# Optimization experiments

Measured on AMD Instinct MI355X. Metric: run time of the kernel, lower is better.

## Reference

```python
import jax, jax.numpy as jnp
import numpy as np

_MAX_SQRT_GRADIENT = 1000.0

@jax.custom_vjp
def sqrt_bound(x):
    return jnp.sqrt(x)

def _sb_fwd(x):
    return jnp.sqrt(x), x

def _sb_bwd(x, g):
    return (g / jnp.sqrt(jnp.maximum(4.0 * x, 1.0 / (_MAX_SQRT_GRADIENT ** 2))),)

sqrt_bound.defvjp(_sb_fwd, _sb_bwd)


def setup_inputs() -> dict:
    B, S, H, L, NH, K = 2, 4096, 2048, 2048, 16, 4
    BW = L // NH
    key = jax.random.key(0)
    ks = jax.random.split(key, 8)
    f = lambda k, shape: jax.random.normal(k, shape, dtype=jnp.float32) * 0.02
    return {
        "input_states": jax.random.normal(ks[0], (B, S, H), dtype=jnp.float32),
        "Wy": f(ks[1], (H, L)), "by": jnp.zeros((L,), jnp.float32),
        "Wx": f(ks[2], (H, L)), "bx": jnp.zeros((L,), jnp.float32),
        "conv_w": f(ks[3], (L, 1, K)), "conv_b": jnp.zeros((L,), jnp.float32),
        "rec_param": f(ks[4], (L,)),
        "igw": f(ks[5], (NH, BW, BW)), "igb": jnp.zeros((NH, BW), jnp.float32),
        "rgw": f(ks[6], (NH, BW, BW)), "rgb": jnp.zeros((NH, BW), jnp.float32),
        "Wout": f(ks[7], (L, H)), "bout": jnp.zeros((H,), jnp.float32),
        "position_ids": jnp.tile(jnp.arange(S, dtype=jnp.int32), (B, 1)),
    }


def reference(input_states, Wy, by, Wx, bx, conv_w, conv_b, rec_param,
              igw, igb, rgw, rgb, Wout, bout, position_ids):
    B, S, H = input_states.shape
    L = Wy.shape[1]
    NH, BW = igw.shape[0], igw.shape[1]
    K = conv_w.shape[-1]

    # y branch: linear + gelu
    y = jax.nn.gelu(input_states @ Wy + by)                      # [B,S,L]

    # x branch: linear + causal depthwise conv1d
    x = input_states @ Wx + bx                                    # [B,S,L]
    xc = jnp.transpose(x, (0, 2, 1))                              # [B,L,S]
    xc = jax.lax.conv_general_dilated(
        xc, conv_w, window_strides=(1,), padding=[(K - 1, 0)],
        dimension_numbers=("NCH", "OIH", "NCH"), feature_group_count=L)
    x = jnp.transpose(xc, (0, 2, 1)) + conv_b                     # [B,S,L]

    # RG-LRU block-diagonal gates
    xh = x.reshape(B, S, NH, BW)
    ig = jax.nn.sigmoid(jnp.einsum("bsnd,nde->bsne", xh, igw) + igb).reshape(B, S, L)
    rg = jax.nn.sigmoid(jnp.einsum("bsnd,nde->bsne", xh, rgw) + rgb).reshape(B, S, L)

    log_a = -8.0 * rg * jax.nn.softplus(rec_param)                # [B,S,L]
    a = jnp.exp(log_a)
    reset = (position_ids == 0)[:, :, None]                       # [B,S,1]

    mult = sqrt_bound(1.0 - jnp.exp(2.0 * log_a))
    mult = jnp.where(reset, 1.0, mult)
    normed = x * ig * mult                                        # [B,S,L]
    a_eff = jnp.where(reset, 0.0, a)                              # [B,S,L]

    def step(h, inp):
        a_t, x_t = inp
        h = a_t.astype(jnp.float32) * h + x_t.astype(jnp.float32)
        return h, h

    h0 = jnp.zeros((B, L), jnp.float32)
    _, hs = jax.lax.scan(step, h0,
                         (jnp.swapaxes(a_eff, 0, 1), jnp.swapaxes(normed, 0, 1)))
    hs = jnp.swapaxes(hs, 0, 1).astype(input_states.dtype)        # [B,S,L]

    return (hs * y) @ Wout + bout                                 # [B,S,H]
```

## Files before the change

### kernel.cpp

```cpp
#include <hip/hip_runtime.h>
#include <cstdint>
#include <cstddef>

#define B_  2
#define S_  4096
#define H_  2048
#define L_  2048
#define NH_ 16
#define M_  (B_*S_)
#define NC_ 64
#define CS_ 64

typedef unsigned short u16;
typedef short  bf8v  __attribute__((ext_vector_type(8)));
typedef u16    u16x8 __attribute__((ext_vector_type(8)));
typedef float  f32x4 __attribute__((ext_vector_type(4)));

__device__ __forceinline__ float bf2f(u16 u){
  union { unsigned i; float f; } v; v.i = ((unsigned)u) << 16; return v.f;
}
__device__ __forceinline__ u16 f2bf(float f){
  union { float f; unsigned i; } v; v.f = f;
  unsigned u = v.i;
  return (u16)((u + 0x7FFFu + ((u >> 16) & 1u)) >> 16);
}
__device__ __forceinline__ void gld16(const void* g, void* l){
  __builtin_amdgcn_global_load_lds((const __attribute__((address_space(1))) void*)g,
                                   (__attribute__((address_space(3))) void*)l, 16, 0, 0);
}

__global__ __launch_bounds__(256)
void gemm_bf16(const u16* __restrict__ A, int lda,
               const u16* __restrict__ Bt, int K,
               const float* __restrict__ bias1, const float* __restrict__ bias2,
               void* __restrict__ C1, u16* __restrict__ C2, int ldc,
               int gelu_flag, int f32out)
{
  __shared__ u16 Alds[128*64];
  __shared__ u16 Blds[128*64];
  const int t    = threadIdx.x;
  const int lane = t & 63;
  const int w    = t >> 6;
  const int wr   = w >> 1, wc = w & 1;
  const int lr   = lane & 15, lk = lane >> 4;

  const int nwg = gridDim.x * gridDim.y;
  const int bid = blockIdx.y * gridDim.x + blockIdx.x;
  const int cpx = nwg >> 3;
  const int swz = (bid & 7) * cpx + (bid >> 3);
  const int bx  = swz % gridDim.x;
  const int by  = swz / gridDim.x;

  const long rowA0 = (long)by * 128;
  const long colB0 = (long)bx * 128;
  const u16* Ag = A  + rowA0 * lda;
  const u16* Bg = Bt + colB0 * K;
  const int srow = t >> 3, scol = t & 7;

#define STAGE(KT) do {                                                     \
    _Pragma("unroll")                                                      \
    for (int it = 0; it < 4; ++it) {                                       \
      int r  = it*32 + srow;                                               \
      int ca = (scol ^ (r & 7)) * 8;                                       \
      gld16(Ag + (long)r*lda + (long)(KT)*64 + ca, Alds + it*2048 + t*8);  \
      gld16(Bg + (long)r*K   + (long)(KT)*64 + ca, Blds + it*2048 + t*8);  \
    } } while(0)

  f32x4 acc[4][4];
#pragma unroll
  for (int m=0;m<4;m++)
#pragma unroll
    for (int n=0;n<4;n++) acc[m][n] = (f32x4){0.f,0.f,0.f,0.f};

  const int nk = K / 64;
  STAGE(0);
  __syncthreads();

  for (int kt = 0; kt < nk; ++kt) {
    bf8v af[4][2], bv[4][2];
#pragma unroll
    for (int m=0;m<4;m++)
#pragma unroll
      for (int ks=0;ks<2;ks++){
        int r  = wr*64 + m*16 + lr;
        int kb = (ks*32 + lk*8)*2;
        af[m][ks] = *(const bf8v*)((const char*)Alds + r*128 + (kb ^ ((r&7)<<4)));
      }
#pragma unroll
    for (int n=0;n<4;n++)
#pragma unroll
      for (int ks=0;ks<2;ks++){
        int r  = wc*64 + n*16 + lr;
        int kb = (ks*32 + lk*8)*2;
        bv[n][ks] = *(const bf8v*)((const char*)Blds + r*128 + (kb ^ ((r&7)<<4)));
      }
    __syncthreads();
    if (kt + 1 < nk) STAGE(kt + 1);
    __builtin_amdgcn_sched_barrier(0);
#pragma unroll
    for (int ks=0;ks<2;ks++)
#pragma unroll
      for (int m=0;m<4;m++)
#pragma unroll
        for (int n=0;n<4;n++)
          acc[m][n] = __builtin_amdgcn_mfma_f32_16x16x32_bf16(af[m][ks], bv[n][ks], acc[m][n], 0, 0, 0);
    if (kt + 1 < nk) __syncthreads();
  }
#undef STAGE

  u16*   Cb = (u16*)C1;
  float* Cf = (float*)C1;
#pragma unroll
  for (int m=0;m<4;m++){
    long row = rowA0 + wr*64 + m*16 + lk*4;
#pragma unroll
    for (int n=0;n<4;n++){
      int col = (int)colB0 + wc*64 + n*16 + lr;
      bool sec = (C2 != nullptr) && (col >= L_);
      float bvv = sec ? bias2[col - L_] : bias1[col];
      bool gel = gelu_flag && !sec;
#pragma unroll
      for (int rr=0; rr<4; ++rr){
        float v = acc[m][n][rr] + bvv;
        if (gel) {
          float u  = 0.7978845608028654f * (v + 0.044715f * v*v*v);
          float tu = fminf(fmaxf(2.f*u, -80.f), 80.f);
          float e  = __expf(tu);
          float th = (e - 1.f) / (e + 1.f);
          v = 0.5f * v * (1.f + th);
        }
        if (sec)          C2[(row+rr)*(long)L_ + (col - L_)] = f2bf(v);
        else if (f32out)  Cf[(row+rr)*(long)ldc + col] = v;
        else              Cb[(row+rr)*(long)ldc + col] = f2bf(v);
      }
    }
  }
}

__global__ __launch_bounds__(256)
void gates_fused(const u16* __restrict__ Xlin, const float* __restrict__ cw,
                 const float* __restrict__ cb, const u16* __restrict__ Gt,
                 const float* __restrict__ gbias, const float* __restrict__ c8,
                 const int* __restrict__ pos,
                 u16* __restrict__ Ae, u16* __restrict__ Nr)
{
  __shared__ __align__(16) char sm[16384 + 32768];
  const int t  = threadIdx.x;
  const int sc = blockIdx.x;
  const int n  = blockIdx.y;
  const int b  = blockIdx.z;
  const int s0 = sc*64;
  const long rowg0 = (long)b*S_ + s0;

  char* xc = sm;
  u16*  xs = (u16*)(sm + 16384);
  char* bs = sm + 16384;

  for (int it=0; it<5; ++it){
    int slot = it*256 + t;
    if (slot < 67*16){
      int i = slot >> 4, c = slot & 15;
      int s = s0 - 3 + i;
      u16x8 v = (u16x8){0,0,0,0,0,0,0,0};
      if (s >= 0)
        v = *(const u16x8*)(Xlin + ((long)b*S_ + s)*L_ + n*128 + c*8);
      *(u16x8*)(xs + i*128 + c*8) = v;
    }
  }
  __syncthreads();

#pragma unroll
  for (int it=0; it<4; ++it){
    int slot = it*256 + t;
    int row = slot >> 4, c = slot & 15;
    int d0 = c*8;
    float a8[8];
#pragma unroll
    for (int j=0;j<8;j++) a8[j] = cb[n*128 + d0 + j];
#pragma unroll
    for (int k=0;k<4;k++){
      u16x8 xv = *(const u16x8*)(xs + (row+k)*128 + d0);
#pragma unroll
      for (int j=0;j<8;j++)
        a8[j] += bf2f(xv[j]) * cw[(n*128 + d0 + j)*4 + k];
    }
    u16x8 o;
#pragma unroll
    for (int j=0;j<8;j++) o[j] = f2bf(a8[j]);
    *(u16x8*)(xc + row*256 + ((d0*2) ^ ((row&7)<<4))) = o;
  }
  __syncthreads();

  const int w  = t >> 6;
  const int lane = t & 63;
  const int lr = lane & 15, lk = lane >> 4;
  const int arow = w*16 + lr;

  bf8v af[4];
#pragma unroll
  for (int ks=0;ks<4;ks++)
    af[ks] = *(const bf8v*)(xc + arow*256 + ((ks*64 + lk*16) ^ ((arow&7)<<4)));

  f32x4 aig[8], brg[8];
#pragma unroll
  for (int half=0; half<2; ++half){
#pragma unroll
    for (int it=0; it<8; ++it){
      int slot = it*256 + t;
      int jr = slot >> 4, c = slot & 15;
      gld16(Gt + (size_t)(n*256 + half*128 + jr)*128 + (size_t)((c ^ (jr&7))*8),
            bs + slot*16);
    }
    __syncthreads();
#pragma unroll
    for (int nf=0; nf<8; ++nf){
      f32x4 acc = (f32x4){0.f,0.f,0.f,0.f};
      int jrow = nf*16 + lr;
#pragma unroll
      for (int ks=0;ks<4;ks++){
        bf8v bv = *(const bf8v*)(bs + jrow*256 + ((ks*64 + lk*16) ^ ((jrow&7)<<4)));
        acc = __builtin_amdgcn_mfma_f32_16x16x32_bf16(af[ks], bv, acc, 0, 0, 0);
      }
      if (half==0) aig[nf] = acc; else brg[nf] = acc;
    }
    __syncthreads();
  }

#pragma unroll
  for (int rr=0; rr<4; ++rr){
    int row = w*16 + lk*4 + rr;
    long gs = rowg0 + row;
    bool reset = (pos[gs] == 0);
#pragma unroll
    for (int nf=0; nf<8; ++nf){
      int dl = nf*16 + lr;
      float ig = 1.f / (1.f + __expf(-(aig[nf][rr] + gbias[n*256 + dl])));
      float rg = 1.f / (1.f + __expf(-(brg[nf][rr] + gbias[n*256 + 128 + dl])));
      float la = c8[n*128 + dl] * rg;
      float a  = __expf(la);
      float mult = reset ? 1.f : sqrtf(fmaxf(1.f - __expf(2.f*la), 0.f));
      u16 xv = *(const u16*)(xc + row*256 + ((dl*2) ^ ((row&7)<<4)));
      float x = bf2f(xv);
      Nr[gs*L_ + n*128 + dl] = f2bf(x * ig * mult);
      Ae[gs*L_ + n*128 + dl] = f2bf(reset ? 0.f : a);
    }
  }
}

__global__ __launch_bounds__(256)
void transpose_cvt(const float* __restrict__ in, u16* __restrict__ out, int R, int C)
{
  __shared__ float tile[64][65];
  int t  = threadIdx.x;
  int tc = blockIdx.x * 64, tr = blockIdx.y * 64;
  int r  = t >> 2, c0 = (t & 3) * 16;
#pragma unroll
  for (int i=0;i<4;i++)
    *(f32x4*)(&tile[r][c0 + i*4]) = *(const f32x4*)(in + (long)(tr+r)*C + tc + c0 + i*4);
  __syncthreads();
  int nl = t >> 2;
#pragma unroll
  for (int it=0; it<2; ++it){
    int g = (t & 3) + it*4;
    u16x8 o;
#pragma unroll
    for (int e=0;e<8;e++) o[e] = f2bf(tile[g*8+e][nl]);
    *(u16x8*)(out + (long)(tc+nl)*R + tr + g*8) = o;
  }
}

__global__ __launch_bounds__(256)
void prep_small(const float* __restrict__ igw, const float* __restrict__ rgw,
                const float* __restrict__ igb, const float* __restrict__ rgb,
                const float* __restrict__ rec, u16* __restrict__ Gt,
                float* __restrict__ gbias, float* __restrict__ c8)
{
  int idx = blockIdx.x*256 + threadIdx.x;
  int d = idx & 127, g = idx >> 7;
  int n = g >> 8, j = g & 255;
  float v = (j < 128) ? igw[(n*128 + d)*128 + j] : rgw[(n*128 + d)*128 + (j-128)];
  Gt[idx] = f2bf(v);
  if (idx < NH_*256) {
    int nn = idx >> 8, jj = idx & 255;
    gbias[idx] = (jj < 128) ? igb[nn*128 + jj] : rgb[nn*128 + jj - 128];
  }
  if (idx < L_) c8[idx] = -8.f * log1pf(__expf(rec[idx]));
}

__global__ __launch_bounds__(256)
void cvt_x(const float* __restrict__ X, u16* __restrict__ Xb)
{
  long idx = (long)blockIdx.x*256 + threadIdx.x;
  f32x4 a = *(const f32x4*)(X + idx*8);
  f32x4 b = *(const f32x4*)(X + idx*8 + 4);
  u16x8 o;
#pragma unroll
  for (int e=0;e<4;e++){ o[e] = f2bf(a[e]); o[4+e] = f2bf(b[e]); }
  *(u16x8*)(Xb + idx*8) = o;
}

__global__ __launch_bounds__(256)
void scan1(const u16* __restrict__ Ae, const u16* __restrict__ Nr,
           float* __restrict__ Ach, float* __restrict__ Hch)
{
  int t = threadIdx.x;
  int l = (blockIdx.x & 7)*256 + t;
  int c = (blockIdx.x >> 3) & (NC_-1);
  int b = blockIdx.x >> 9;
  long base = ((long)b*S_ + (long)c*CS_)*L_ + l;
  float A = 1.f, h = 0.f;
#pragma unroll 8
  for (int s=0; s<CS_; ++s){
    float a = bf2f(Ae[base + (long)s*L_]);
    float x = bf2f(Nr[base + (long)s*L_]);
    h = fmaf(a, h, x);
    A *= a;
  }
  long o = ((long)b*NC_ + c)*L_ + l;
  Ach[o] = A; Hch[o] = h;
}

__global__ __launch_bounds__(256)
void scan2(const float* __restrict__ Ach, const float* __restrict__ Hch,
           float* __restrict__ Hcar)
{
  int idx = blockIdx.x*256 + threadIdx.x;
  int b = idx >> 11, l = idx & (L_-1);
  float h = 0.f;
  for (int c=0; c<NC_; ++c){
    long o = ((long)b*NC_ + c)*L_ + l;
    Hcar[o] = h;
    h = fmaf(Ach[o], h, Hch[o]);
  }
}

__global__ __launch_bounds__(256)
void scan3(const u16* __restrict__ Ae, const u16* __restrict__ Nr,
           const float* __restrict__ Hcar, const u16* __restrict__ Y,
           u16* __restrict__ Z)
{
  int t = threadIdx.x;
  int l = (blockIdx.x & 7)*256 + t;
  int c = (blockIdx.x >> 3) & (NC_-1);
  int b = blockIdx.x >> 9;
  long base = ((long)b*S_ + (long)c*CS_)*L_ + l;
  float h = Hcar[((long)b*NC_ + c)*L_ + l];
#pragma unroll 8
  for (int s=0; s<CS_; ++s){
    long o = base + (long)s*L_;
    h = fmaf(bf2f(Ae[o]), h, bf2f(Nr[o]));
    Z[o] = f2bf(h * bf2f(Y[o]));
  }
}

extern "C" void kernel_launch(void* const* d_in, const int* in_sizes, int n_in,
                              void* d_out, int out_size, void* d_ws, size_t ws_size,
                              hipStream_t stream)
{
  (void)in_sizes; (void)n_in; (void)out_size; (void)ws_size;
  const float* X    = (const float*)d_in[0];
  const float* Wy   = (const float*)d_in[1];
  const float* by   = (const float*)d_in[2];
  const float* Wx   = (const float*)d_in[3];
  const float* bx   = (const float*)d_in[4];
  const float* cw   = (const float*)d_in[5];
  const float* cb   = (const float*)d_in[6];
  const float* rec  = (const float*)d_in[7];
  const float* igw  = (const float*)d_in[8];
  const float* igb  = (const float*)d_in[9];
  const float* rgw  = (const float*)d_in[10];
  const float* rgb  = (const float*)d_in[11];
  const float* Wout = (const float*)d_in[12];
  const float* bout = (const float*)d_in[13];
  const int*   pos  = (const int*)d_in[14];
  float* out = (float*)d_out;

  char* ws = (char*)d_ws;
  size_t o_Xbf  = 0;
  size_t o_Xlin = o_Xbf  + (size_t)M_*H_*2;
  size_t o_WyT  = o_Xlin + (size_t)M_*L_*2;
  size_t o_WxT  = o_WyT  + (size_t)H_*L_*2;
  size_t o_WoT  = o_WxT  + (size_t)H_*L_*2;
  size_t o_Gt   = o_WoT  + (size_t)L_*H_*2;
  size_t o_gb   = o_Gt   + (size_t)NH_*256*128*2;
  size_t o_c8   = o_gb   + 4096*4;
  size_t o_Y    = o_c8   + 2048*4;
  size_t o_xc   = o_Y    + (size_t)M_*L_*2;
  size_t o_Ae   = o_xc   + (size_t)M_*L_*2;
  size_t o_Nr   = o_Ae   + (size_t)M_*L_*2;
  size_t o_Ach  = o_Nr   + (size_t)M_*L_*2;
  size_t o_Hch  = o_Ach  + (size_t)B_*NC_*L_*4;
  size_t o_Hca  = o_Hch  + (size_t)B_*NC_*L_*4;

  u16*   Xbf   = (u16*)(ws + o_Xbf);
  u16*   Xlin  = (u16*)(ws + o_Xlin);
  u16*   WyT   = (u16*)(ws + o_WyT);
  u16*   WxT   = (u16*)(ws + o_WxT);
  u16*   WoT   = (u16*)(ws + o_WoT);
  u16*   Gt    = (u16*)(ws + o_Gt);
  float* gbias = (float*)(ws + o_gb);
  float* c8    = (float*)(ws + o_c8);
  u16*   Y     = (u16*)(ws + o_Y);
  u16*   Z     = (u16*)(ws + o_xc);
  u16*   Ae    = (u16*)(ws + o_Ae);
  u16*   Nr    = (u16*)(ws + o_Nr);
  float* Ach   = (float*)(ws + o_Ach);
  float* Hch   = (float*)(ws + o_Hch);
  float* Hcar  = (float*)(ws + o_Hca);

  dim3 blk(256);
  transpose_cvt<<<dim3(32,32), blk, 0, stream>>>(Wy,  WyT, 2048, 2048);
  transpose_cvt<<<dim3(32,32), blk, 0, stream>>>(Wx,  WxT, 2048, 2048);
  transpose_cvt<<<dim3(32,32), blk, 0, stream>>>(Wout,WoT, 2048, 2048);
  prep_small<<<dim3(2048), blk, 0, stream>>>(igw, rgw, igb, rgb, rec, Gt, gbias, c8);
  cvt_x<<<dim3(8192), blk, 0, stream>>>(X, Xbf);
  gemm_bf16<<<dim3(32,64), blk, 0, stream>>>(Xbf, H_, WyT, H_, by, bx, Y, Xlin, L_, 1, 0);
  gates_fused<<<dim3(NC_, NH_, B_), blk, 0, stream>>>(Xlin, cw, cb, Gt, gbias, c8, pos, Ae, Nr);
  scan1<<<dim3(1024), blk, 0, stream>>>(Ae, Nr, Ach, Hch);
  scan2<<<dim3(16),   blk, 0, stream>>>(Ach, Hch, Hcar);
  scan3<<<dim3(1024), blk, 0, stream>>>(Ae, Nr, Hcar, Y, Z);
  gemm_bf16<<<dim3(16,64), blk, 0, stream>>>(Z, L_, WoT, L_, bout, bout, out, nullptr, H_, 0, 1);
}
```

Baseline: 456.7 us.

## Fuse chunk scan summaries into gates kernel and fold carry scan into scan3

The gates kernel now computes per-chunk (A, h) scan summaries in registers, combining them with wave shuffles and shared memory, so the separate scan1 pass that re-read Ae and Nr is removed. scan2 is also removed: each scan3 block recomputes its carry-in serially over the preceding chunk summaries. The three weight transposes are merged into one launch. This cuts a full read of two large bf16 arrays and two kernel launches, at the cost of redundant carry work in scan3 that grows with chunk index.

Measured after the change: 424.0 us. -7.2%, faster.

```diff
diff --git a/kernel.cpp b/kernel.cpp
--- a/kernel.cpp
+++ b/kernel.cpp
@@ -24,6 +24,7 @@
   unsigned u = v.i;
   return (u16)((u + 0x7FFFu + ((u >> 16) & 1u)) >> 16);
 }
+__device__ __forceinline__ float bfr(float f){ return bf2f(f2bf(f)); }
 __device__ __forceinline__ void gld16(const void* g, void* l){
   __builtin_amdgcn_global_load_lds((const __attribute__((address_space(1))) void*)g,
                                    (__attribute__((address_space(3))) void*)l, 16, 0, 0);
@@ -142,7 +143,8 @@
                  const float* __restrict__ cb, const u16* __restrict__ Gt,
                  const float* __restrict__ gbias, const float* __restrict__ c8,
                  const int* __restrict__ pos,
-                 u16* __restrict__ Ae, u16* __restrict__ Nr)
+                 u16* __restrict__ Ae, u16* __restrict__ Nr,
+                 float* __restrict__ Ach, float* __restrict__ Hch)
 {
   __shared__ __align__(16) char sm[16384 + 32768];
   const int t  = threadIdx.x;
@@ -226,30 +228,75 @@
     __syncthreads();
   }
 
-#pragma unroll
-  for (int rr=0; rr<4; ++rr){
-    int row = w*16 + lk*4 + rr;
-    long gs = rowg0 + row;
-    bool reset = (pos[gs] == 0);
-#pragma unroll
-    for (int nf=0; nf<8; ++nf){
-      int dl = nf*16 + lr;
-      float ig = 1.f / (1.f + __expf(-(aig[nf][rr] + gbias[n*256 + dl])));
-      float rg = 1.f / (1.f + __expf(-(brg[nf][rr] + gbias[n*256 + 128 + dl])));
-      float la = c8[n*128 + dl] * rg;
+  float* wsA = (float*)bs;
+  float* wsh = (float*)(bs + 2048);
+  bool rst[4];
+#pragma unroll
+  for (int rr=0; rr<4; ++rr) rst[rr] = (pos[rowg0 + w*16 + lk*4 + rr] == 0);
+
+#pragma unroll
+  for (int nf=0; nf<8; ++nf){
+    int dl = nf*16 + lr;
+    float gb1 = gbias[n*256 + dl];
+    float gb2 = gbias[n*256 + 128 + dl];
+    float cc8 = c8[n*128 + dl];
+    float Aseg = 1.f, hseg = 0.f;
+#pragma unroll
+    for (int rr=0; rr<4; ++rr){
+      int row = w*16 + lk*4 + rr;
+      long gs = rowg0 + row;
+      float ig = 1.f / (1.f + __expf(-(aig[nf][rr] + gb1)));
+      float rg = 1.f / (1.f + __expf(-(brg[nf][rr] + gb2)));
+      float la = cc8 * rg;
       float a  = __expf(la);
-      float mult = reset ? 1.f : sqrtf(fmaxf(1.f - __expf(2.f*la), 0.f));
+      float mult = rst[rr] ? 1.f : sqrtf(fmaxf(1.f - __expf(2.f*la), 0.f));
       u16 xv = *(const u16*)(xc + row*256 + ((dl*2) ^ ((row&7)<<4)));
       float x = bf2f(xv);
-      Nr[gs*L_ + n*128 + dl] = f2bf(x * ig * mult);
-      Ae[gs*L_ + n*128 + dl] = f2bf(reset ? 0.f : a);
-    }
-  }
-}
-
-__global__ __launch_bounds__(256)
-void transpose_cvt(const float* __restrict__ in, u16* __restrict__ out, int R, int C)
-{
+      float nrv = bfr(x * ig * mult);
+      float aev = rst[rr] ? 0.f : bfr(a);
+      Nr[gs*L_ + n*128 + dl] = f2bf(nrv);
+      Ae[gs*L_ + n*128 + dl] = f2bf(aev);
+      hseg = fmaf(aev, hseg, nrv);
+      Aseg *= aev;
+    }
+    {
+      float Ap = __shfl_xor(Aseg, 16);
+      float hp = __shfl_xor(hseg, 16);
+      bool low = ((lk & 1) == 0);
+      float Alo = low ? Aseg : Ap, Ahi = low ? Ap : Aseg;
+      float hlo = low ? hseg : hp, hhi = low ? hp : hseg;
+      Aseg = Alo * Ahi; hseg = fmaf(Ahi, hlo, hhi);
+      Ap = __shfl_xor(Aseg, 32);
+      hp = __shfl_xor(hseg, 32);
+      low = ((lk & 2) == 0);
+      Alo = low ? Aseg : Ap; Ahi = low ? Ap : Aseg;
+      hlo = low ? hseg : hp; hhi = low ? hp : hseg;
+      Aseg = Alo * Ahi; hseg = fmaf(Ahi, hlo, hhi);
+    }
+    if (lk == 0){ wsA[w*128 + dl] = Aseg; wsh[w*128 + dl] = hseg; }
+  }
+  __syncthreads();
+  if (t < 128){
+    float A = wsA[t], h = wsh[t];
+#pragma unroll
+    for (int ww=1; ww<4; ++ww){
+      float Aw = wsA[ww*128 + t], hw = wsh[ww*128 + t];
+      h = fmaf(Aw, h, hw);
+      A *= Aw;
+    }
+    long o = ((long)b*NC_ + sc)*L_ + n*128 + t;
+    Ach[o] = A; Hch[o] = h;
+  }
+}
+
+__global__ __launch_bounds__(256)
+void transpose_cvt3(const float* __restrict__ s0, const float* __restrict__ s1,
+                    const float* __restrict__ s2, u16* __restrict__ d0,
+                    u16* __restrict__ d1, u16* __restrict__ d2)
+{
+  const float* in  = (blockIdx.z == 0) ? s0 : (blockIdx.z == 1) ? s1 : s2;
+  u16*         out = (blockIdx.z == 0) ? d0 : (blockIdx.z == 1) ? d1 : d2;
+  const int R = 2048, C = 2048;
   __shared__ float tile[64][65];
   int t  = threadIdx.x;
   int tc = blockIdx.x * 64, tr = blockIdx.y * 64;
@@ -300,51 +347,20 @@
 }
 
 __global__ __launch_bounds__(256)
-void scan1(const u16* __restrict__ Ae, const u16* __restrict__ Nr,
-           float* __restrict__ Ach, float* __restrict__ Hch)
+void scan3(const u16* __restrict__ Ae, const u16* __restrict__ Nr,
+           const float* __restrict__ Ach, const float* __restrict__ Hch,
+           const u16* __restrict__ Y, u16* __restrict__ Z)
 {
   int t = threadIdx.x;
   int l = (blockIdx.x & 7)*256 + t;
   int c = (blockIdx.x >> 3) & (NC_-1);
   int b = blockIdx.x >> 9;
+  float h = 0.f;
+  for (int cc = 0; cc < c; ++cc){
+    long o = ((long)b*NC_ + cc)*L_ + l;
+    h = fmaf(Ach[o], h, Hch[o]);
+  }
   long base = ((long)b*S_ + (long)c*CS_)*L_ + l;
-  float A = 1.f, h = 0.f;
-#pragma unroll 8
-  for (int s=0; s<CS_; ++s){
-    float a = bf2f(Ae[base + (long)s*L_]);
-    float x = bf2f(Nr[base + (long)s*L_]);
-    h = fmaf(a, h, x);
-    A *= a;
-  }
-  long o = ((long)b*NC_ + c)*L_ + l;
-  Ach[o] = A; Hch[o] = h;
-}
-
-__global__ __launch_bounds__(256)
-void scan2(const float* __restrict__ Ach, const float* __restrict__ Hch,
-           float* __restrict__ Hcar)
-{
-  int idx = blockIdx.x*256 + threadIdx.x;
-  int b = idx >> 11, l = idx & (L_-1);
-  float h = 0.f;
-  for (int c=0; c<NC_; ++c){
-    long o = ((long)b*NC_ + c)*L_ + l;
-    Hcar[o] = h;
-    h = fmaf(Ach[o], h, Hch[o]);
-  }
-}
-
-__global__ __launch_bounds__(256)
-void scan3(const u16* __restrict__ Ae, const u16* __restrict__ Nr,
-           const float* __restrict__ Hcar, const u16* __restrict__ Y,
-           u16* __restrict__ Z)
-{
-  int t = threadIdx.x;
-  int l = (blockIdx.x & 7)*256 + t;
-  int c = (blockIdx.x >> 3) & (NC_-1);
-  int b = blockIdx.x >> 9;
-  long base = ((long)b*S_ + (long)c*CS_)*L_ + l;
-  float h = Hcar[((long)b*NC_ + c)*L_ + l];
 #pragma unroll 8
   for (int s=0; s<CS_; ++s){
     long o = base + (long)s*L_;
@@ -390,7 +406,6 @@
   size_t o_Nr   = o_Ae   + (size_t)M_*L_*2;
   size_t o_Ach  = o_Nr   + (size_t)M_*L_*2;
   size_t o_Hch  = o_Ach  + (size_t)B_*NC_*L_*4;
-  size_t o_Hca  = o_Hch  + (size_t)B_*NC_*L_*4;
 
   u16*   Xbf   = (u16*)(ws + o_Xbf);
   u16*   Xlin  = (u16*)(ws + o_Xlin);
@@ -406,18 +421,14 @@
   u16*   Nr    = (u16*)(ws + o_Nr);
   float* Ach   = (float*)(ws + o_Ach);
   float* Hch   = (float*)(ws + o_Hch);
-  float* Hcar  = (float*)(ws + o_Hca);
 
   dim3 blk(256);
-  transpose_cvt<<<dim3(32,32), blk, 0, stream>>>(Wy,  WyT, 2048, 2048);
-  transpose_cvt<<<dim3(32,32), blk, 0, stream>>>(Wx,  WxT, 2048, 2048);
-  transpose_cvt<<<dim3(32,32), blk, 0, stream>>>(Wout,WoT, 2048, 2048);
+  transpose_cvt3<<<dim3(32,32,3), blk, 0, stream>>>(Wy, Wx, Wout, WyT, WxT, WoT);
   prep_small<<<dim3(2048), blk, 0, stream>>>(igw, rgw, igb, rgb, rec, Gt, gbias, c8);
   cvt_x<<<dim3(8192), blk, 0, stream>>>(X, Xbf);
   gemm_bf16<<<dim3(32,64), blk, 0, stream>>>(Xbf, H_, WyT, H_, by, bx, Y, Xlin, L_, 1, 0);
-  gates_fused<<<dim3(NC_, NH_, B_), blk, 0, stream>>>(Xlin, cw, cb, Gt, gbias, c8, pos, Ae, Nr);
-  scan1<<<dim3(1024), blk, 0, stream>>>(Ae, Nr, Ach, Hch);
-  scan2<<<dim3(16),   blk, 0, stream>>>(Ach, Hch, Hcar);
-  scan3<<<dim3(1024), blk, 0, stream>>>(Ae, Nr, Hcar, Y, Z);
+  gates_fused<<<dim3(NC_, NH_, B_), blk, 0, stream>>>(Xlin, cw, cb, Gt, gbias, c8, pos,
+                                                      Ae, Nr, Ach, Hch);
+  scan3<<<dim3(1024), blk, 0, stream>>>(Ae, Nr, Ach, Hch, Y, Z);
   gemm_bf16<<<dim3(16,64), blk, 0, stream>>>(Z, L_, WoT, L_, bout, bout, out, nullptr, H_, 0, 1);
 }
```
